# Kernel optimization log

Hardware: AMD Instinct MI355X
Metric: run time of the kernel (lower is better)

Reference implementation:

```python
import jax, jax.numpy as jnp
import numpy as np

N_NODES = 5000
N_EDGES = 160000
HID = 64
NODE_F = 4
TASK_F = 4
BATCH = 512


def _glorot(key, shape):
    fan_in = shape[-1]
    return jax.random.normal(key, shape, dtype=jnp.float32) / jnp.sqrt(jnp.float32(fan_in))


def setup_inputs() -> dict:
    key = jax.random.key(0)
    ks = jax.random.split(key, 16)
    x = jax.random.normal(ks[0], (N_NODES, NODE_F), dtype=jnp.float32)
    edge_index = jax.random.randint(ks[1], (2, N_EDGES), 0, N_NODES, dtype=jnp.int64)
    task_feat = jax.random.normal(ks[2], (BATCH, TASK_F), dtype=jnp.float32)
    return {
        "x": x,
        "edge_index": edge_index,
        "task_feat": task_feat,
        # SAGEConv layer 1: out = lin_l(mean_neigh) + lin_r(x); lin_l has bias, lin_r (root) has no bias (PyG default)
        "Wl1": _glorot(ks[3], (HID, NODE_F)), "bl1": jnp.zeros((HID,), jnp.float32),
        "Wr1": _glorot(ks[4], (HID, NODE_F)),
        # SAGEConv layer 2
        "Wl2": _glorot(ks[5], (HID, HID)), "bl2": jnp.zeros((HID,), jnp.float32),
        "Wr2": _glorot(ks[6], (HID, HID)),
        # task_encoder: Linear(4,64) -> ReLU -> Linear(64,64)
        "Wt1": _glorot(ks[7], (HID, TASK_F)), "bt1": jnp.zeros((HID,), jnp.float32),
        "Wt2": _glorot(ks[8], (HID, HID)), "bt2": jnp.zeros((HID,), jnp.float32),
        # classifier: Linear(128,64) -> ReLU -> Linear(64,1)
        "Wc1": _glorot(ks[9], (HID, 2 * HID)), "bc1": jnp.zeros((HID,), jnp.float32),
        "Wc2": _glorot(ks[10], (1, HID)), "bc2": jnp.zeros((1,), jnp.float32),
    }


def _sage_conv(x, src, dst, Wl, bl, Wr):
    # PyG SAGEConv(mean): messages flow src -> dst; mean over incoming neighbors
    msg_sum = jax.ops.segment_sum(x[src], dst, num_segments=N_NODES)
    deg = jax.ops.segment_sum(jnp.ones((src.shape[0],), x.dtype), dst, num_segments=N_NODES)
    mean_neigh = msg_sum / jnp.maximum(deg, 1.0)[:, None]
    return mean_neigh @ Wl.T + bl + x @ Wr.T


def reference(x, edge_index, task_feat,
              Wl1, bl1, Wr1, Wl2, bl2, Wr2,
              Wt1, bt1, Wt2, bt2, Wc1, bc1, Wc2, bc2):
    src, dst = edge_index[0], edge_index[1]
    h = jax.nn.relu(_sage_conv(x, src, dst, Wl1, bl1, Wr1))        # [N, HID]
    h = jax.nn.relu(_sage_conv(h, src, dst, Wl2, bl2, Wr2))        # [N, HID]
    t = jax.nn.relu(task_feat @ Wt1.T + bt1) @ Wt2.T + bt2         # [B, HID]
    # classifier on concat([h, t]) == split Wc1 into h-part and t-part; avoids materializing the concat
    h_part = h @ Wc1[:, :HID].T                                    # [N, HID]
    t_part = t @ Wc1[:, HID:].T + bc1                              # [B, HID]
    hidden = jax.nn.relu(h_part[None, :, :] + t_part[:, None, :])  # [B, N, HID]
    scores = jnp.einsum('bnh,h->bn', hidden, Wc2[0]) + bc2[0]      # [B, N]
    return scores
```

## Files before the change

### kernel.cpp

```cpp
#include <hip/hip_runtime.h>

#define N_NODES 5000
#define N_EDGES 160000
#define HID 64
#define BATCH 512
#define CSTRIDE 96


__global__ __launch_bounds__(256) void zero_kernel(int* __restrict__ cnt) {
    int i = blockIdx.x * 256 + threadIdx.x;
    if (i < N_NODES) cnt[i] = 0;
}

__global__ __launch_bounds__(256) void build_kernel(
        const int* __restrict__ ei, const float* __restrict__ task_feat,
        const float* __restrict__ Wt1, const float* __restrict__ bt1,
        const float* __restrict__ Wt2, const float* __restrict__ bt2,
        const float* __restrict__ Wc1, const float* __restrict__ bc1,
        const float* __restrict__ Wl1, const float* __restrict__ Wr1,
        const float* __restrict__ Wl2, const float* __restrict__ Wr2,
        int* __restrict__ cnt, int* __restrict__ compact, float* __restrict__ t_part,
        float* __restrict__ Wl1T, float* __restrict__ Wr1T,
        float* __restrict__ Wl2T, float* __restrict__ Wr2T,
        float* __restrict__ Wc1hT) {
    int tid = threadIdx.x;
    int blk = blockIdx.x;
    __shared__ float s1[4][64];
    __shared__ float s2[4][64];

    if (blk < 625) {
        int e = blk * 256 + tid;
        int src = ei[e];
        int dst = ei[N_EDGES + e];
        int q = atomicAdd(&cnt[dst], 1);
        if (q < CSTRIDE) compact[dst * CSTRIDE + q] = src;
    } else if (blk < 629) {
        int w = blk - 625;
        if (w == 0) {
            for (int idx = tid; idx < 4096; idx += 256) {
                int k = idx >> 6, h = idx & 63;
                Wl2T[idx] = Wl2[h * 64 + k];
            }
        } else if (w == 1) {
            for (int idx = tid; idx < 4096; idx += 256) {
                int k = idx >> 6, h = idx & 63;
                Wr2T[idx] = Wr2[h * 64 + k];
            }
        } else if (w == 2) {
            for (int idx = tid; idx < 4096; idx += 256) {
                int k = idx >> 6, h = idx & 63;
                Wc1hT[idx] = Wc1[h * 128 + k];
            }
        } else {
            int k = tid >> 6, h = tid & 63;
            Wl1T[tid] = Wl1[h * 4 + k];
            Wr1T[tid] = Wr1[h * 4 + k];
        }
    } else {
        int grp = tid >> 6, h = tid & 63;
        int b = (blk - 629) * 4 + grp;
        float4 tf = ((const float4*)task_feat)[b];
        float4 w1 = ((const float4*)Wt1)[h];
        float v = bt1[h] + tf.x * w1.x + tf.y * w1.y + tf.z * w1.z + tf.w * w1.w;
        s1[grp][h] = fmaxf(v, 0.f);
        __syncthreads();
        const float4* w2r = (const float4*)(Wt2 + h * 64);
        const float4* s1v = (const float4*)s1[grp];
        float v2 = bt2[h];
#pragma unroll
        for (int q = 0; q < 16; q++) {
            float4 w = w2r[q]; float4 ss = s1v[q];
            v2 += ss.x * w.x + ss.y * w.y + ss.z * w.z + ss.w * w.w;
        }
        s2[grp][h] = v2;
        __syncthreads();
        const float4* wcr = (const float4*)(Wc1 + h * 128 + 64);
        const float4* s2v = (const float4*)s2[grp];
        float p = bc1[h];
#pragma unroll
        for (int q = 0; q < 16; q++) {
            float4 w = wcr[q]; float4 ss = s2v[q];
            p += ss.x * w.x + ss.y * w.y + ss.z * w.z + ss.w * w.w;
        }
        t_part[b * 64 + h] = p;
    }
}

__global__ __launch_bounds__(256) void layer1_kernel(
        const float* __restrict__ x, const int* __restrict__ cnt,
        const int* __restrict__ compact,
        const float* __restrict__ Wl1T, const float* __restrict__ bl1,
        const float* __restrict__ Wr1T, float* __restrict__ h1) {
    int lane = threadIdx.x & 63, grp = threadIdx.x >> 6;
    int n = blockIdx.x * 4 + grp;
    int d = min(cnt[n], CSTRIDE);
    const int* row = compact + n * CSTRIDE;
    float4 xs = make_float4(0.f, 0.f, 0.f, 0.f);
    if (lane < d) {
        float4 xv = ((const float4*)x)[row[lane]];
        xs.x += xv.x; xs.y += xv.y; xs.z += xv.z; xs.w += xv.w;
    }
    if (lane + 64 < d) {
        float4 xv = ((const float4*)x)[row[lane + 64]];
        xs.x += xv.x; xs.y += xv.y; xs.z += xv.z; xs.w += xv.w;
    }
#pragma unroll
    for (int off = 1; off < 64; off <<= 1) {
        xs.x += __shfl_xor(xs.x, off);
        xs.y += __shfl_xor(xs.y, off);
        xs.z += __shfl_xor(xs.z, off);
        xs.w += __shfl_xor(xs.w, off);
    }
    float inv = 1.f / fmaxf((float)d, 1.f);
    float m0 = xs.x * inv, m1 = xs.y * inv, m2 = xs.z * inv, m3 = xs.w * inv;
    float4 xn = ((const float4*)x)[n];
    float v = bl1[lane]
            + m0 * Wl1T[lane] + m1 * Wl1T[64 + lane]
            + m2 * Wl1T[128 + lane] + m3 * Wl1T[192 + lane]
            + xn.x * Wr1T[lane] + xn.y * Wr1T[64 + lane]
            + xn.z * Wr1T[128 + lane] + xn.w * Wr1T[192 + lane];
    h1[n * 64 + lane] = fmaxf(v, 0.f);
}

__global__ __launch_bounds__(256) void layer2_kernel(
        const float* __restrict__ h1, const int* __restrict__ cnt,
        const int* __restrict__ compact,
        const float* __restrict__ Wl2T, const float* __restrict__ bl2,
        const float* __restrict__ Wr2T, const float* __restrict__ Wc1hT,
        float* __restrict__ h_part) {
    int h = threadIdx.x & 63, grp = threadIdx.x >> 6;
    int n = blockIdx.x * 4 + grp;
    int d = min(cnt[n], CSTRIDE);
    const int* bucket = compact + n * CSTRIDE;
    float a0 = 0.f, a1 = 0.f, a2 = 0.f, a3 = 0.f;
    int j = 0;
    for (; j + 4 <= d; j += 4) {
        int e0 = bucket[j], e1 = bucket[j + 1], e2 = bucket[j + 2], e3 = bucket[j + 3];
        a0 += h1[e0 * 64 + h];
        a1 += h1[e1 * 64 + h];
        a2 += h1[e2 * 64 + h];
        a3 += h1[e3 * 64 + h];
    }
    for (; j < d; j++) a0 += h1[bucket[j] * 64 + h];
    float m = (a0 + a1 + a2 + a3) / fmaxf((float)d, 1.f);

    __shared__ float shm[4][64], shh[4][64], shh2[4][64];
    shm[grp][h] = m;
    shh[grp][h] = h1[n * 64 + h];
    __syncthreads();
    float v = bl2[h];
#pragma unroll
    for (int k = 0; k < 64; k++)
        v += shm[grp][k] * Wl2T[k * 64 + h] + shh[grp][k] * Wr2T[k * 64 + h];
    shh2[grp][h] = fmaxf(v, 0.f);
    __syncthreads();
    float p = 0.f;
#pragma unroll
    for (int k = 0; k < 64; k++) p += shh2[grp][k] * Wc1hT[k * 64 + h];
    h_part[n * 64 + h] = p;
}

__global__ __launch_bounds__(256) void scores_kernel(
        const float* __restrict__ h_part, const float* __restrict__ t_part,
        const float* __restrict__ Wc2, const float* __restrict__ bc2,
        float* __restrict__ out) {
    int tid = threadIdx.x;
    int n = blockIdx.x * 256 + tid;
    bool valid = n < N_NODES;
    int nn = valid ? n : (N_NODES - 1);
    float hr[64];
    const float4* hp = (const float4*)(h_part + nn * 64);
#pragma unroll
    for (int i = 0; i < 16; i++) {
        float4 v = hp[i];
        hr[4 * i + 0] = v.x; hr[4 * i + 1] = v.y;
        hr[4 * i + 2] = v.z; hr[4 * i + 3] = v.w;
    }
    float b2 = bc2[0];
    int b0 = blockIdx.y * 8;
    for (int bb = 0; bb < 8; bb++) {
        const float* tp = t_part + (b0 + bb) * 64;
        float acc0 = 0.f, acc1 = 0.f, acc2 = 0.f, acc3 = 0.f;
#pragma unroll
        for (int h = 0; h < 64; h += 4) {
            acc0 = fmaf(fmaxf(hr[h + 0] + tp[h + 0], 0.f), Wc2[h + 0], acc0);
            acc1 = fmaf(fmaxf(hr[h + 1] + tp[h + 1], 0.f), Wc2[h + 1], acc1);
            acc2 = fmaf(fmaxf(hr[h + 2] + tp[h + 2], 0.f), Wc2[h + 2], acc2);
            acc3 = fmaf(fmaxf(hr[h + 3] + tp[h + 3], 0.f), Wc2[h + 3], acc3);
        }
        if (valid)
            out[(b0 + bb) * N_NODES + n] = (acc0 + acc1) + (acc2 + acc3) + b2;
    }
}

extern "C" void kernel_launch(void* const* d_in, const int* in_sizes, int n_in,
                              void* d_out, int out_size, void* d_ws, size_t ws_size,
                              hipStream_t stream) {
    const float* x    = (const float*)d_in[0];
    const int*   ei   = (const int*)d_in[1];
    const float* task = (const float*)d_in[2];
    const float* Wl1  = (const float*)d_in[3];
    const float* bl1  = (const float*)d_in[4];
    const float* Wr1  = (const float*)d_in[5];
    const float* Wl2  = (const float*)d_in[6];
    const float* bl2  = (const float*)d_in[7];
    const float* Wr2  = (const float*)d_in[8];
    const float* Wt1  = (const float*)d_in[9];
    const float* bt1  = (const float*)d_in[10];
    const float* Wt2  = (const float*)d_in[11];
    const float* bt2  = (const float*)d_in[12];
    const float* Wc1  = (const float*)d_in[13];
    const float* bc1  = (const float*)d_in[14];
    const float* Wc2  = (const float*)d_in[15];
    const float* bc2  = (const float*)d_in[16];
    float* out = (float*)d_out;

    char* ws = (char*)d_ws;
    int*   cnt     = (int*)(ws + 0);
    int*   compact = (int*)(ws + 20000);
    float* h1      = (float*)(ws + 1940000);
    float* h_part  = (float*)(ws + 3220000);
    float* t_part  = (float*)(ws + 4500000);
    float* Wl1T  = (float*)(ws + 4631072);
    float* Wr1T  = (float*)(ws + 4632096);
    float* Wl2T  = (float*)(ws + 4633120);
    float* Wr2T  = (float*)(ws + 4649504);
    float* Wc1hT = (float*)(ws + 4665888);

    zero_kernel<<<(N_NODES + 255) / 256, 256, 0, stream>>>(cnt);
    build_kernel<<<625 + 4 + BATCH / 4, 256, 0, stream>>>(
        ei, task, Wt1, bt1, Wt2, bt2, Wc1, bc1, Wl1, Wr1, Wl2, Wr2,
        cnt, compact, t_part, Wl1T, Wr1T, Wl2T, Wr2T, Wc1hT);
    layer1_kernel<<<N_NODES / 4, 256, 0, stream>>>(x, cnt, compact, Wl1T, bl1, Wr1T, h1);
    layer2_kernel<<<N_NODES / 4, 256, 0, stream>>>(h1, cnt, compact, Wl2T, bl2, Wr2T,
                                                   Wc1hT, h_part);
    scores_kernel<<<dim3(20, 64), 256, 0, stream>>>(h_part, t_part, Wc2, bc2, out);
}
```

Baseline: 150.7 us.

## Fuse build, layer, and score kernels into one persistent kernel with grid barriers

Merges the build, layer1, layer2 and scores kernels into one persistent kernel of 512 blocks. The stages are separated by software grid barriers built from atomic counters in workspace memory. The goal is to remove the launch gaps and tail effects between the four dependent launches. The cost is atomic spin-wait barriers and grid-stride loops. Correctness relies on all 512 blocks being resident at once, which the launch bounds of 2 blocks per SIMD group make plausible on a 256-CU part.

```diff
diff --git a/kernel.cpp b/kernel.cpp
--- a/kernel.cpp
+++ b/kernel.cpp
@@ -5,191 +5,206 @@
 #define HID 64
 #define BATCH 512
 #define CSTRIDE 96
-
-
-__global__ __launch_bounds__(256) void zero_kernel(int* __restrict__ cnt) {
+#define G 512
+#define NT (G * 256)
+#define NWAVES (G * 4)
+#define NODE_ITERS 3
+
+
+__global__ __launch_bounds__(256) void zero_kernel(int* __restrict__ cnt,
+                                                   int* __restrict__ bar) {
     int i = blockIdx.x * 256 + threadIdx.x;
     if (i < N_NODES) cnt[i] = 0;
-}
-
-__global__ __launch_bounds__(256) void build_kernel(
-        const int* __restrict__ ei, const float* __restrict__ task_feat,
+    if (i < 4) bar[i] = 0;
+}
+
+__device__ inline void gbar(int* __restrict__ bar, int idx) {
+    __syncthreads();
+    if (threadIdx.x == 0) {
+        __threadfence();
+        atomicAdd(&bar[idx], 1);
+        while (atomicAdd(&bar[idx], 0) < G)
+            __builtin_amdgcn_s_sleep(1);
+        __threadfence();
+    }
+    __syncthreads();
+}
+
+__global__ __launch_bounds__(256, 2) void fused_kernel(
+        const float* __restrict__ x, const int* __restrict__ ei,
+        const float* __restrict__ task_feat,
+        const float* __restrict__ Wl1, const float* __restrict__ bl1,
+        const float* __restrict__ Wr1,
+        const float* __restrict__ Wl2, const float* __restrict__ bl2,
+        const float* __restrict__ Wr2,
         const float* __restrict__ Wt1, const float* __restrict__ bt1,
         const float* __restrict__ Wt2, const float* __restrict__ bt2,
         const float* __restrict__ Wc1, const float* __restrict__ bc1,
-        const float* __restrict__ Wl1, const float* __restrict__ Wr1,
-        const float* __restrict__ Wl2, const float* __restrict__ Wr2,
-        int* __restrict__ cnt, int* __restrict__ compact, float* __restrict__ t_part,
+        const float* __restrict__ Wc2, const float* __restrict__ bc2,
+        int* __restrict__ cnt, int* __restrict__ compact,
+        float* __restrict__ h1, float* __restrict__ h_part,
+        float* __restrict__ t_part,
         float* __restrict__ Wl1T, float* __restrict__ Wr1T,
         float* __restrict__ Wl2T, float* __restrict__ Wr2T,
-        float* __restrict__ Wc1hT) {
-    int tid = threadIdx.x;
-    int blk = blockIdx.x;
-    __shared__ float s1[4][64];
-    __shared__ float s2[4][64];
-
-    if (blk < 625) {
-        int e = blk * 256 + tid;
+        float* __restrict__ Wc1hT, int* __restrict__ bar,
+        float* __restrict__ out) {
+    int tid  = threadIdx.x;
+    int blk  = blockIdx.x;
+    int gid  = blk * 256 + tid;
+    int lane = tid & 63, grp = tid >> 6;
+    int w    = blk * 4 + grp;
+
+    __shared__ union SM {
+        struct { float s1[4][64]; float s2[4][64]; } t;
+        struct { float m[4][64]; float h[4][64]; float h2[4][64]; } l2;
+    } sm;
+
+    for (int e = gid; e < N_EDGES; e += NT) {
         int src = ei[e];
         int dst = ei[N_EDGES + e];
         int q = atomicAdd(&cnt[dst], 1);
         if (q < CSTRIDE) compact[dst * CSTRIDE + q] = src;
-    } else if (blk < 629) {
-        int w = blk - 625;
-        if (w == 0) {
-            for (int idx = tid; idx < 4096; idx += 256) {
-                int k = idx >> 6, h = idx & 63;
-                Wl2T[idx] = Wl2[h * 64 + k];
-            }
-        } else if (w == 1) {
-            for (int idx = tid; idx < 4096; idx += 256) {
-                int k = idx >> 6, h = idx & 63;
-                Wr2T[idx] = Wr2[h * 64 + k];
-            }
-        } else if (w == 2) {
-            for (int idx = tid; idx < 4096; idx += 256) {
-                int k = idx >> 6, h = idx & 63;
-                Wc1hT[idx] = Wc1[h * 128 + k];
-            }
-        } else {
-            int k = tid >> 6, h = tid & 63;
-            Wl1T[tid] = Wl1[h * 4 + k];
-            Wr1T[tid] = Wr1[h * 4 + k];
-        }
-    } else {
-        int grp = tid >> 6, h = tid & 63;
-        int b = (blk - 629) * 4 + grp;
+    }
+    if (gid < 4096) {
+        Wl2T[gid] = Wl2[(gid & 63) * 64 + (gid >> 6)];
+    } else if (gid < 8192) {
+        int idx = gid - 4096;
+        Wr2T[idx] = Wr2[(idx & 63) * 64 + (idx >> 6)];
+    } else if (gid < 12288) {
+        int idx = gid - 8192;
+        Wc1hT[idx] = Wc1[(idx & 63) * 128 + (idx >> 6)];
+    } else if (gid < 12544) {
+        int idx = gid - 12288;
+        Wl1T[idx] = Wl1[(idx & 63) * 4 + (idx >> 6)];
+        Wr1T[idx] = Wr1[(idx & 63) * 4 + (idx >> 6)];
+    }
+    if (blk < BATCH / 4) {
+        int b = blk * 4 + grp, h = lane;
         float4 tf = ((const float4*)task_feat)[b];
         float4 w1 = ((const float4*)Wt1)[h];
         float v = bt1[h] + tf.x * w1.x + tf.y * w1.y + tf.z * w1.z + tf.w * w1.w;
-        s1[grp][h] = fmaxf(v, 0.f);
+        sm.t.s1[grp][h] = fmaxf(v, 0.f);
         __syncthreads();
         const float4* w2r = (const float4*)(Wt2 + h * 64);
-        const float4* s1v = (const float4*)s1[grp];
+        const float4* s1v = (const float4*)sm.t.s1[grp];
         float v2 = bt2[h];
 #pragma unroll
         for (int q = 0; q < 16; q++) {
-            float4 w = w2r[q]; float4 ss = s1v[q];
-            v2 += ss.x * w.x + ss.y * w.y + ss.z * w.z + ss.w * w.w;
-        }
-        s2[grp][h] = v2;
+            float4 ww = w2r[q]; float4 ss = s1v[q];
+            v2 += ss.x * ww.x + ss.y * ww.y + ss.z * ww.z + ss.w * ww.w;
+        }
+        sm.t.s2[grp][h] = v2;
         __syncthreads();
         const float4* wcr = (const float4*)(Wc1 + h * 128 + 64);
-        const float4* s2v = (const float4*)s2[grp];
+        const float4* s2v = (const float4*)sm.t.s2[grp];
         float p = bc1[h];
 #pragma unroll
         for (int q = 0; q < 16; q++) {
-            float4 w = wcr[q]; float4 ss = s2v[q];
-            p += ss.x * w.x + ss.y * w.y + ss.z * w.z + ss.w * w.w;
+            float4 ww = wcr[q]; float4 ss = s2v[q];
+            p += ss.x * ww.x + ss.y * ww.y + ss.z * ww.z + ss.w * ww.w;
         }
         t_part[b * 64 + h] = p;
     }
-}
-
-__global__ __launch_bounds__(256) void layer1_kernel(
-        const float* __restrict__ x, const int* __restrict__ cnt,
-        const int* __restrict__ compact,
-        const float* __restrict__ Wl1T, const float* __restrict__ bl1,
-        const float* __restrict__ Wr1T, float* __restrict__ h1) {
-    int lane = threadIdx.x & 63, grp = threadIdx.x >> 6;
-    int n = blockIdx.x * 4 + grp;
-    int d = min(cnt[n], CSTRIDE);
-    const int* row = compact + n * CSTRIDE;
-    float4 xs = make_float4(0.f, 0.f, 0.f, 0.f);
-    if (lane < d) {
-        float4 xv = ((const float4*)x)[row[lane]];
-        xs.x += xv.x; xs.y += xv.y; xs.z += xv.z; xs.w += xv.w;
-    }
-    if (lane + 64 < d) {
-        float4 xv = ((const float4*)x)[row[lane + 64]];
-        xs.x += xv.x; xs.y += xv.y; xs.z += xv.z; xs.w += xv.w;
-    }
-#pragma unroll
-    for (int off = 1; off < 64; off <<= 1) {
-        xs.x += __shfl_xor(xs.x, off);
-        xs.y += __shfl_xor(xs.y, off);
-        xs.z += __shfl_xor(xs.z, off);
-        xs.w += __shfl_xor(xs.w, off);
-    }
-    float inv = 1.f / fmaxf((float)d, 1.f);
-    float m0 = xs.x * inv, m1 = xs.y * inv, m2 = xs.z * inv, m3 = xs.w * inv;
-    float4 xn = ((const float4*)x)[n];
-    float v = bl1[lane]
-            + m0 * Wl1T[lane] + m1 * Wl1T[64 + lane]
-            + m2 * Wl1T[128 + lane] + m3 * Wl1T[192 + lane]
-            + xn.x * Wr1T[lane] + xn.y * Wr1T[64 + lane]
-            + xn.z * Wr1T[128 + lane] + xn.w * Wr1T[192 + lane];
-    h1[n * 64 + lane] = fmaxf(v, 0.f);
-}
-
-__global__ __launch_bounds__(256) void layer2_kernel(
-        const float* __restrict__ h1, const int* __restrict__ cnt,
-        const int* __restrict__ compact,
-        const float* __restrict__ Wl2T, const float* __restrict__ bl2,
-        const float* __restrict__ Wr2T, const float* __restrict__ Wc1hT,
-        float* __restrict__ h_part) {
-    int h = threadIdx.x & 63, grp = threadIdx.x >> 6;
-    int n = blockIdx.x * 4 + grp;
-    int d = min(cnt[n], CSTRIDE);
-    const int* bucket = compact + n * CSTRIDE;
-    float a0 = 0.f, a1 = 0.f, a2 = 0.f, a3 = 0.f;
-    int j = 0;
-    for (; j + 4 <= d; j += 4) {
-        int e0 = bucket[j], e1 = bucket[j + 1], e2 = bucket[j + 2], e3 = bucket[j + 3];
-        a0 += h1[e0 * 64 + h];
-        a1 += h1[e1 * 64 + h];
-        a2 += h1[e2 * 64 + h];
-        a3 += h1[e3 * 64 + h];
-    }
-    for (; j < d; j++) a0 += h1[bucket[j] * 64 + h];
-    float m = (a0 + a1 + a2 + a3) / fmaxf((float)d, 1.f);
-
-    __shared__ float shm[4][64], shh[4][64], shh2[4][64];
-    shm[grp][h] = m;
-    shh[grp][h] = h1[n * 64 + h];
-    __syncthreads();
-    float v = bl2[h];
-#pragma unroll
-    for (int k = 0; k < 64; k++)
-        v += shm[grp][k] * Wl2T[k * 64 + h] + shh[grp][k] * Wr2T[k * 64 + h];
-    shh2[grp][h] = fmaxf(v, 0.f);
-    __syncthreads();
-    float p = 0.f;
-#pragma unroll
-    for (int k = 0; k < 64; k++) p += shh2[grp][k] * Wc1hT[k * 64 + h];
-    h_part[n * 64 + h] = p;
-}
-
-__global__ __launch_bounds__(256) void scores_kernel(
-        const float* __restrict__ h_part, const float* __restrict__ t_part,
-        const float* __restrict__ Wc2, const float* __restrict__ bc2,
-        float* __restrict__ out) {
-    int tid = threadIdx.x;
-    int n = blockIdx.x * 256 + tid;
-    bool valid = n < N_NODES;
-    int nn = valid ? n : (N_NODES - 1);
-    float hr[64];
-    const float4* hp = (const float4*)(h_part + nn * 64);
-#pragma unroll
-    for (int i = 0; i < 16; i++) {
-        float4 v = hp[i];
-        hr[4 * i + 0] = v.x; hr[4 * i + 1] = v.y;
-        hr[4 * i + 2] = v.z; hr[4 * i + 3] = v.w;
-    }
+    gbar(bar, 0);
+
+    for (int it = 0; it < NODE_ITERS; ++it) {
+        int n = w + it * NWAVES;
+        if (n < N_NODES) {
+            int d = min(cnt[n], CSTRIDE);
+            const int* row = compact + n * CSTRIDE;
+            float4 xs = make_float4(0.f, 0.f, 0.f, 0.f);
+            if (lane < d) {
+                float4 xv = ((const float4*)x)[row[lane]];
+                xs.x += xv.x; xs.y += xv.y; xs.z += xv.z; xs.w += xv.w;
+            }
+            if (lane + 64 < d) {
+                float4 xv = ((const float4*)x)[row[lane + 64]];
+                xs.x += xv.x; xs.y += xv.y; xs.z += xv.z; xs.w += xv.w;
+            }
+#pragma unroll
+            for (int off = 1; off < 64; off <<= 1) {
+                xs.x += __shfl_xor(xs.x, off);
+                xs.y += __shfl_xor(xs.y, off);
+                xs.z += __shfl_xor(xs.z, off);
+                xs.w += __shfl_xor(xs.w, off);
+            }
+            float inv = 1.f / fmaxf((float)d, 1.f);
+            float m0 = xs.x * inv, m1 = xs.y * inv, m2 = xs.z * inv, m3 = xs.w * inv;
+            float4 xn = ((const float4*)x)[n];
+            float v = bl1[lane]
+                    + m0 * Wl1T[lane] + m1 * Wl1T[64 + lane]
+                    + m2 * Wl1T[128 + lane] + m3 * Wl1T[192 + lane]
+                    + xn.x * Wr1T[lane] + xn.y * Wr1T[64 + lane]
+                    + xn.z * Wr1T[128 + lane] + xn.w * Wr1T[192 + lane];
+            h1[n * 64 + lane] = fmaxf(v, 0.f);
+        }
+    }
+    gbar(bar, 1);
+
+    for (int it = 0; it < NODE_ITERS; ++it) {
+        int n = w + it * NWAVES;
+        bool valid = n < N_NODES;
+        int nn = valid ? n : 0;
+        int h = lane;
+        int d = valid ? min(cnt[nn], CSTRIDE) : 0;
+        const int* bucket = compact + nn * CSTRIDE;
+        float a0 = 0.f, a1 = 0.f, a2 = 0.f, a3 = 0.f;
+        int j = 0;
+        for (; j + 4 <= d; j += 4) {
+            int e0 = bucket[j], e1 = bucket[j + 1], e2 = bucket[j + 2], e3 = bucket[j + 3];
+            a0 += h1[e0 * 64 + h];
+            a1 += h1[e1 * 64 + h];
+            a2 += h1[e2 * 64 + h];
+            a3 += h1[e3 * 64 + h];
+        }
+        for (; j < d; j++) a0 += h1[bucket[j] * 64 + h];
+        float m = (a0 + a1 + a2 + a3) / fmaxf((float)d, 1.f);
+
+        sm.l2.m[grp][h] = m;
+        sm.l2.h[grp][h] = h1[nn * 64 + h];
+        __syncthreads();
+        float v = bl2[h];
+#pragma unroll
+        for (int k = 0; k < 64; k++)
+            v += sm.l2.m[grp][k] * Wl2T[k * 64 + h] + sm.l2.h[grp][k] * Wr2T[k * 64 + h];
+        sm.l2.h2[grp][h] = fmaxf(v, 0.f);
+        __syncthreads();
+        float p = 0.f;
+#pragma unroll
+        for (int k = 0; k < 64; k++) p += sm.l2.h2[grp][k] * Wc1hT[k * 64 + h];
+        if (valid) h_part[n * 64 + h] = p;
+        __syncthreads();
+    }
+    gbar(bar, 2);
+
     float b2 = bc2[0];
-    int b0 = blockIdx.y * 8;
-    for (int bb = 0; bb < 8; bb++) {
-        const float* tp = t_part + (b0 + bb) * 64;
-        float acc0 = 0.f, acc1 = 0.f, acc2 = 0.f, acc3 = 0.f;
-#pragma unroll
-        for (int h = 0; h < 64; h += 4) {
-            acc0 = fmaf(fmaxf(hr[h + 0] + tp[h + 0], 0.f), Wc2[h + 0], acc0);
-            acc1 = fmaf(fmaxf(hr[h + 1] + tp[h + 1], 0.f), Wc2[h + 1], acc1);
-            acc2 = fmaf(fmaxf(hr[h + 2] + tp[h + 2], 0.f), Wc2[h + 2], acc2);
-            acc3 = fmaf(fmaxf(hr[h + 3] + tp[h + 3], 0.f), Wc2[h + 3], acc3);
-        }
-        if (valid)
-            out[(b0 + bb) * N_NODES + n] = (acc0 + acc1) + (acc2 + acc3) + b2;
+    for (int p = blk; p < 20 * 64; p += G) {
+        int bt = p / 20, ntile = p - bt * 20;
+        int n = ntile * 256 + tid;
+        bool valid = n < N_NODES;
+        int nn = valid ? n : (N_NODES - 1);
+        float hr[64];
+        const float4* hp = (const float4*)(h_part + nn * 64);
+#pragma unroll
+        for (int i = 0; i < 16; i++) {
+            float4 v = hp[i];
+            hr[4 * i + 0] = v.x; hr[4 * i + 1] = v.y;
+            hr[4 * i + 2] = v.z; hr[4 * i + 3] = v.w;
+        }
+        int b0 = bt * 8;
+        for (int bb = 0; bb < 8; bb++) {
+            const float* tp = t_part + (b0 + bb) * 64;
+            float acc0 = 0.f, acc1 = 0.f, acc2 = 0.f, acc3 = 0.f;
+#pragma unroll
+            for (int h = 0; h < 64; h += 4) {
+                acc0 = fmaf(fmaxf(hr[h + 0] + tp[h + 0], 0.f), Wc2[h + 0], acc0);
+                acc1 = fmaf(fmaxf(hr[h + 1] + tp[h + 1], 0.f), Wc2[h + 1], acc1);
+                acc2 = fmaf(fmaxf(hr[h + 2] + tp[h + 2], 0.f), Wc2[h + 2], acc2);
+                acc3 = fmaf(fmaxf(hr[h + 3] + tp[h + 3], 0.f), Wc2[h + 3], acc3);
+            }
+            if (valid)
+                out[(b0 + bb) * N_NODES + n] = (acc0 + acc1) + (acc2 + acc3) + b2;
+        }
     }
 }
 
@@ -226,13 +241,12 @@
     float* Wl2T  = (float*)(ws + 4633120);
     float* Wr2T  = (float*)(ws + 4649504);
     float* Wc1hT = (float*)(ws + 4665888);
-
-    zero_kernel<<<(N_NODES + 255) / 256, 256, 0, stream>>>(cnt);
-    build_kernel<<<625 + 4 + BATCH / 4, 256, 0, stream>>>(
-        ei, task, Wt1, bt1, Wt2, bt2, Wc1, bc1, Wl1, Wr1, Wl2, Wr2,
-        cnt, compact, t_part, Wl1T, Wr1T, Wl2T, Wr2T, Wc1hT);
-    layer1_kernel<<<N_NODES / 4, 256, 0, stream>>>(x, cnt, compact, Wl1T, bl1, Wr1T, h1);
-    layer2_kernel<<<N_NODES / 4, 256, 0, stream>>>(h1, cnt, compact, Wl2T, bl2, Wr2T,
-                                                   Wc1hT, h_part);
-    scores_kernel<<<dim3(20, 64), 256, 0, stream>>>(h_part, t_part, Wc2, bc2, out);
-}
+    int*   bar   = (int*)(ws + 4682272);
+
+    zero_kernel<<<(N_NODES + 255) / 256, 256, 0, stream>>>(cnt, bar);
+    fused_kernel<<<G, 256, 0, stream>>>(
+        x, ei, task, Wl1, bl1, Wr1, Wl2, bl2, Wr2,
+        Wt1, bt1, Wt2, bt2, Wc1, bc1, Wc2, bc2,
+        cnt, compact, h1, h_part, t_part,
+        Wl1T, Wr1T, Wl2T, Wr2T, Wc1hT, bar, out);
+}
```

Result: slower. 376.3 us (+149.6%).
